# Kernel optimization log

Hardware: AMD Instinct MI355X
Metric: run time of the kernel (lower is better)

## Reference

```python
import jax, jax.numpy as jnp
import numpy as np
from jax import lax

PAD = 40
MAX_DISP = 40
STRIDE2 = 1
CORR_MULT = 1.0


def _correlation1d(input1, input2):
    # input1, input2: [B, C, H, W]; kernel_size=1, stride1=1
    B, C, H, W = input1.shape
    D = 2 * MAX_DISP // STRIDE2 + 1  # 81 displacement channels
    # zero-pad input2 along the width dimension
    in2p = jnp.pad(input2, ((0, 0), (0, 0), (0, 0), (PAD, PAD)))
    offsets = jnp.arange(D, dtype=jnp.int32) * STRIDE2  # start col in padded map; disp = off - PAD

    def body(carry, off):
        shifted = lax.dynamic_slice(in2p, (0, 0, 0, off), (B, C, H, W))
        # mean over channels (sumelems = kernel_size^2 * C = C)
        c = jnp.sum(input1 * shifted, axis=1) / C  # [B, H, W]
        return carry, c

    _, corr = lax.scan(body, None, offsets)  # [D, B, H, W]
    out = jnp.transpose(corr, (1, 0, 2, 3)) * CORR_MULT  # [B, D, H, W]
    return out


def setup_inputs() -> dict:
    key = jax.random.key(0)
    k1, k2 = jax.random.split(key)
    input1 = jax.random.normal(k1, (8, 256, 96, 192), dtype=jnp.float32)
    input2 = jax.random.normal(k2, (8, 256, 96, 192), dtype=jnp.float32)
    return {"input1": input1, "input2": input2}


def reference(input1, input2):
    return _correlation1d(input1, input2)
```

## Files before the change

kernel.cpp:

```cpp
#include <hip/hip_runtime.h>


typedef __attribute__((ext_vector_type(8))) short short8;
typedef __attribute__((ext_vector_type(4))) short short4v;
typedef __attribute__((ext_vector_type(4))) float float4v;

#if defined(__has_builtin)
#if __has_builtin(__builtin_amdgcn_mfma_f32_16x16x16bf16_1k)
#define HAVE_MFMA16 1
#endif
#endif
#ifndef HAVE_MFMA16
#define HAVE_MFMA16 0
#endif

__device__ __forceinline__ unsigned short f2bf(float f) {
  unsigned int u = __float_as_uint(f);
  return (unsigned short)((u + 0x7FFFu + ((u >> 16) & 1u)) >> 16);
}

__device__ __forceinline__ void glds4(const float* g, float* l) {
  __builtin_amdgcn_global_load_lds(
      (const __attribute__((address_space(1))) void*)g,
      (__attribute__((address_space(3))) void*)l, 4, 0, 0);
}

__global__ __launch_bounds__(256, 3) void corr1d_kernel(
    const float* __restrict__ in1, const float* __restrict__ in2,
    float* __restrict__ out) {
  constexpr int W = 192, H = 96, C = 256, D = 81;
  constexpr int HW = H * W;
  constexpr int KC = 16;
  constexpr int SR = 194;
  constexpr int ES = 196;
  constexpr int BUF = KC * SR;

  __shared__ __align__(16) float smem[4 * BUF];
  float* E = smem;

  const int bh = blockIdx.x;
  const int b = bh / H, h = bh % H;
  const int tid = threadIdx.x;
  const int lane = tid & 63;
  const int wv = tid >> 6;
  const int l15 = lane & 15, lq = lane >> 4;
  const int base = (b * C * H + h) * W;

  float4v acc[3][6];
#pragma unroll
  for (int i = 0; i < 3; ++i)
#pragma unroll
    for (int jj = 0; jj < 6; ++jj) acc[i][jj] = (float4v){0.f, 0.f, 0.f, 0.f};

  auto stage = [&](int m, int p) {
    const int c0 = KC * m;
    float* As = smem + p * (2 * BUF);
    float* Bs = As + BUF;
#pragma unroll
    for (int r = 0; r < 4; ++r) {
      const int k = 4 * wv + r;
      const float* g1 = in1 + base + (c0 + k) * HW + lane;
      const float* g2 = in2 + base + (c0 + k) * HW + lane;
      float* lA = As + k * SR;
      float* lB = Bs + k * SR;
#pragma unroll
      for (int g = 0; g < 3; ++g) {
        glds4(g1 + 64 * g, lA + 64 * g);
        glds4(g2 + 64 * g, lB + 64 * g);
      }
    }
  };

  auto compute_chunk = [&](int p) {
    const float* As = smem + p * (2 * BUF);
    const float* Bs = As + BUF;
#if HAVE_MFMA16
    short4v af[3];
#pragma unroll
    for (int i = 0; i < 3; ++i) {
      const float* ap = As + 48 * wv + 16 * i + l15;
      unsigned short o[4];
#pragma unroll
      for (int t = 0; t < 4; ++t) o[t] = f2bf(ap[(4 * lq + t) * SR]);
      af[i] = *(const short4v*)o;
    }
#pragma unroll
    for (int jt = 0; jt < 8; ++jt) {
      const int j = 16 * (3 * wv + jt) + l15;
      const bool ok = (j >= 40) && (j < 232);
      const float* bp = Bs + (ok ? (j - 40) : 0);
      unsigned short o[4];
#pragma unroll
      for (int t = 0; t < 4; ++t) {
        float v = ok ? bp[(4 * lq + t) * SR] : 0.0f;
        o[t] = f2bf(v);
      }
      short4v bfr = *(const short4v*)o;
#pragma unroll
      for (int i = 0; i < 3; ++i) {
        const int jj = jt - i;
        if (jj >= 0 && jj < 6)
          acc[i][jj] = __builtin_amdgcn_mfma_f32_16x16x16bf16_1k(
              af[i], bfr, acc[i][jj], 0, 0, 0);
      }
    }
#else
    const bool okq = (lq < 2);
    const int rb = okq ? 8 * lq : 0;
    short8 af[3];
#pragma unroll
    for (int i = 0; i < 3; ++i) {
      const float* ap = As + 48 * wv + 16 * i + l15;
      unsigned short o[8];
#pragma unroll
      for (int t = 0; t < 8; ++t) {
        float v = ap[(rb + t) * SR];
        o[t] = okq ? f2bf(v) : (unsigned short)0;
      }
      af[i] = *(const short8*)o;
    }
#pragma unroll
    for (int jt = 0; jt < 8; ++jt) {
      const int j = 16 * (3 * wv + jt) + l15;
      const bool ok = (j >= 40) && (j < 232);
      const float* bp = Bs + (ok ? (j - 40) : 0);
      unsigned short o[8];
#pragma unroll
      for (int t = 0; t < 8; ++t) {
        float v = bp[(rb + t) * SR];
        o[t] = (ok && okq) ? f2bf(v) : (unsigned short)0;
      }
      short8 bfr = *(const short8*)o;
#pragma unroll
      for (int i = 0; i < 3; ++i) {
        const int jj = jt - i;
        if (jj >= 0 && jj < 6)
          acc[i][jj] = __builtin_amdgcn_mfma_f32_16x16x32_bf16(
              af[i], bfr, acc[i][jj], 0, 0, 0);
      }
    }
#endif
  };

  stage(0, 0);
#pragma unroll 1
  for (int t7 = 0; t7 < 7; ++t7) {
    stage(2 * t7 + 1, 1);
    asm volatile("s_waitcnt vmcnt(24)" ::: "memory");
    __builtin_amdgcn_s_barrier();
    compute_chunk(0);
    __builtin_amdgcn_s_barrier();
    stage(2 * t7 + 2, 0);
    asm volatile("s_waitcnt vmcnt(24)" ::: "memory");
    __builtin_amdgcn_s_barrier();
    compute_chunk(1);
    __builtin_amdgcn_s_barrier();
  }
  stage(15, 1);
  asm volatile("s_waitcnt vmcnt(24)" ::: "memory");
  __builtin_amdgcn_s_barrier();
  compute_chunk(0);
  __builtin_amdgcn_s_barrier();
  asm volatile("s_waitcnt vmcnt(0)" ::: "memory");
  __builtin_amdgcn_s_barrier();
  compute_chunk(1);

  const float scale = 1.0f / 256.0f;
#pragma unroll
  for (int p = 0; p < 2; ++p) {
    const int dlo = p ? 41 : 0;
    const int nd  = p ? 40 : 41;
    __syncthreads();
#pragma unroll
    for (int i = 0; i < 3; ++i)
#pragma unroll
      for (int jj = 0; jj < 6; ++jj)
#pragma unroll
        for (int r = 0; r < 4; ++r) {
          const int d = 16 * jj + l15 - 4 * lq - r;
          const int w = 48 * wv + 16 * i + 4 * lq + r;
          if (d >= dlo && d < dlo + nd)
            E[(d - dlo) * ES + w] = acc[i][jj][r] * scale;
        }
    __syncthreads();
    for (int t = tid; t < nd * 48; t += 256) {
      const int dr = t / 48, g = t % 48;
      float4v val = *(const float4v*)(E + dr * ES + 4 * g);
      *(float4v*)(out + ((b * D + dlo + dr) * H + h) * W + 4 * g) = val;
    }
  }
}

extern "C" void kernel_launch(void* const* d_in, const int* in_sizes, int n_in,
                              void* d_out, int out_size, void* d_ws, size_t ws_size,
                              hipStream_t stream) {
  const float* in1 = (const float*)d_in[0];
  const float* in2 = (const float*)d_in[1];
  float* out = (float*)d_out;
  (void)in_sizes; (void)n_in; (void)out_size; (void)d_ws; (void)ws_size;
  corr1d_kernel<<<dim3(768), dim3(256), 0, stream>>>(in1, in2, out);
}
```

Before: 325.0 us.

## Stage inputs via vectorized register loads with double-buffered prefetch into LDS

Replaces the per-dword global_load_lds staging with 16-byte vector global loads into two register buffers, which are then written to LDS. Loads run two chunks ahead of compute, with explicit vmcnt/lgkmcnt waits around the barriers. The LDS row stride is padded to 196 so the 16-byte LDS stores stay aligned. This is meant to cut the number of load instructions and hide global latency. The cost is many extra VGPRs for the staging buffers, which under the 3-blocks-per-CU launch bound may cause spills or lower occupancy.

```diff
diff --git a/kernel.cpp b/kernel.cpp
--- a/kernel.cpp
+++ b/kernel.cpp
@@ -17,12 +17,6 @@
 __device__ __forceinline__ unsigned short f2bf(float f) {
   unsigned int u = __float_as_uint(f);
   return (unsigned short)((u + 0x7FFFu + ((u >> 16) & 1u)) >> 16);
-}
-
-__device__ __forceinline__ void glds4(const float* g, float* l) {
-  __builtin_amdgcn_global_load_lds(
-      (const __attribute__((address_space(1))) void*)g,
-      (__attribute__((address_space(3))) void*)l, 4, 0, 0);
 }
 
 __global__ __launch_bounds__(256, 3) void corr1d_kernel(
@@ -31,7 +25,7 @@
   constexpr int W = 192, H = 96, C = 256, D = 81;
   constexpr int HW = H * W;
   constexpr int KC = 16;
-  constexpr int SR = 194;
+  constexpr int SR = 196;
   constexpr int ES = 196;
   constexpr int BUF = KC * SR;
 
@@ -52,22 +46,53 @@
 #pragma unroll
     for (int jj = 0; jj < 6; ++jj) acc[i][jj] = (float4v){0.f, 0.f, 0.f, 0.f};
 
-  auto stage = [&](int m, int p) {
-    const int c0 = KC * m;
-    float* As = smem + p * (2 * BUF);
-    float* Bs = As + BUF;
-#pragma unroll
-    for (int r = 0; r < 4; ++r) {
-      const int k = 4 * wv + r;
-      const float* g1 = in1 + base + (c0 + k) * HW + lane;
-      const float* g2 = in2 + base + (c0 + k) * HW + lane;
-      float* lA = As + k * SR;
-      float* lB = Bs + k * SR;
-#pragma unroll
-      for (int g = 0; g < 3; ++g) {
-        glds4(g1 + 64 * g, lA + 64 * g);
-        glds4(g2 + 64 * g, lB + 64 * g);
-      }
+  int soff[3], loff[3];
+#pragma unroll
+  for (int g = 0; g < 3; ++g) {
+    const int fidx = 256 * g + 4 * lane;
+    const int r = fidx / 192;
+    const int col = fidx - 192 * r;
+    soff[g] = (4 * wv + r) * HW + col;
+    loff[g] = (4 * wv + r) * SR + col;
+  }
+  const float* in1p = in1 + base;
+  const float* in2p = in2 + base;
+
+  float4v rA0[3], rB0[3], rA1[3], rB1[3];
+  auto LOAD0 = [&](int m) {
+    const float* g1 = in1p + KC * m * HW;
+    const float* g2 = in2p + KC * m * HW;
+#pragma unroll
+    for (int g = 0; g < 3; ++g) {
+      rA0[g] = *(const float4v*)(g1 + soff[g]);
+      rB0[g] = *(const float4v*)(g2 + soff[g]);
+    }
+  };
+  auto LOAD1 = [&](int m) {
+    const float* g1 = in1p + KC * m * HW;
+    const float* g2 = in2p + KC * m * HW;
+#pragma unroll
+    for (int g = 0; g < 3; ++g) {
+      rA1[g] = *(const float4v*)(g1 + soff[g]);
+      rB1[g] = *(const float4v*)(g2 + soff[g]);
+    }
+  };
+  auto WRITE0 = [&]() {
+    float* As = smem;
+    float* Bs = smem + BUF;
+#pragma unroll
+    for (int g = 0; g < 3; ++g) {
+      *(float4v*)(As + loff[g]) = rA0[g];
+      *(float4v*)(Bs + loff[g]) = rB0[g];
+    }
+  };
+  auto WRITE1 = [&]() {
+    float* As = smem + 2 * BUF;
+    float* Bs = smem + 3 * BUF;
+#pragma unroll
+    for (int g = 0; g < 3; ++g) {
+      *(float4v*)(As + loff[g]) = rA1[g];
+      *(float4v*)(Bs + loff[g]) = rB1[g];
     }
   };
 
@@ -142,26 +167,36 @@
 #endif
   };
 
-  stage(0, 0);
+  LOAD0(0);
+  LOAD1(1);
+  asm volatile("s_waitcnt vmcnt(6)" ::: "memory");
+  WRITE0();
+  LOAD0(2);
+  asm volatile("s_waitcnt lgkmcnt(0)" ::: "memory");
+  __builtin_amdgcn_s_barrier();
 #pragma unroll 1
-  for (int t7 = 0; t7 < 7; ++t7) {
-    stage(2 * t7 + 1, 1);
-    asm volatile("s_waitcnt vmcnt(24)" ::: "memory");
-    __builtin_amdgcn_s_barrier();
+  for (int t = 0; t < 7; ++t) {
+    const int m = 2 * t;
     compute_chunk(0);
     __builtin_amdgcn_s_barrier();
-    stage(2 * t7 + 2, 0);
-    asm volatile("s_waitcnt vmcnt(24)" ::: "memory");
+    asm volatile("s_waitcnt vmcnt(6)" ::: "memory");
+    WRITE1();
+    if (m + 3 < 16) LOAD1(m + 3);
+    asm volatile("s_waitcnt lgkmcnt(0)" ::: "memory");
     __builtin_amdgcn_s_barrier();
     compute_chunk(1);
     __builtin_amdgcn_s_barrier();
+    asm volatile("s_waitcnt vmcnt(6)" ::: "memory");
+    WRITE0();
+    if (m + 4 < 16) LOAD0(m + 4);
+    asm volatile("s_waitcnt lgkmcnt(0)" ::: "memory");
+    __builtin_amdgcn_s_barrier();
   }
-  stage(15, 1);
-  asm volatile("s_waitcnt vmcnt(24)" ::: "memory");
-  __builtin_amdgcn_s_barrier();
   compute_chunk(0);
   __builtin_amdgcn_s_barrier();
   asm volatile("s_waitcnt vmcnt(0)" ::: "memory");
+  WRITE1();
+  asm volatile("s_waitcnt lgkmcnt(0)" ::: "memory");
   __builtin_amdgcn_s_barrier();
   compute_chunk(1);
 
```

After: 331.9 us. +2.1%, slower.
